# Performance work log

Measured on AMD Instinct MI355X. Metric: run time of the kernel, lower is better.

Reference implementation:

```python
import jax, jax.numpy as jnp
import numpy as np

B, N, E = 2, 32768, 32768
DIM = 3
MP_STEPS = 2
H = 32  # hidden width; original bug: depth == hidden width (range(hidden))


def _ln(x, g, b):
    m = jnp.mean(x, axis=-1, keepdims=True)
    v = jnp.var(x, axis=-1, keepdims=True)
    return (x - m) * jax.lax.rsqrt(v + 1e-5) * g + b


def _mlp(x, Win, bin_, Wh, bh, Wout, bout, lng=None, lnb=None):
    # Linear -> ReLU -> [LN] -> H x (Linear -> ReLU -> [LN]) -> Linear -> ReLU
    h = jax.nn.relu(x @ Win + bin_)
    if lng is not None:
        h = _ln(h, lng[0], lnb[0])
        def body(h, p):
            W, b_, g_, bb = p
            return _ln(jax.nn.relu(h @ W + b_), g_, bb), None
        h, _ = jax.lax.scan(body, h, (Wh, bh, lng[1:], lnb[1:]))
    else:
        def body(h, p):
            W, b_ = p
            return jax.nn.relu(h @ W + b_), None
        h, _ = jax.lax.scan(body, h, (Wh, bh))
    return jax.nn.relu(h @ Wout + bout)


def _mk(key, din, h, dout, ln, pref):
    ks = jax.random.split(key, 3)
    d = {
        pref + 'Win': jax.random.normal(ks[0], (din, h), jnp.float32) / np.sqrt(din).astype(np.float32),
        pref + 'bin': jnp.zeros((h,), jnp.float32),
        pref + 'Wh': jax.random.normal(ks[1], (h, h, h), jnp.float32) / np.sqrt(h).astype(np.float32),
        pref + 'bh': jnp.zeros((h, h), jnp.float32),
        pref + 'Wout': jax.random.normal(ks[2], (h, dout), jnp.float32) / np.sqrt(h).astype(np.float32),
        pref + 'bout': jnp.zeros((dout,), jnp.float32),
    }
    if ln:
        d[pref + 'lng'] = jnp.ones((h + 1, h), jnp.float32)
        d[pref + 'lnb'] = jnp.zeros((h + 1, h), jnp.float32)
    return d


def setup_inputs() -> dict:
    key = jax.random.key(0)
    ks = jax.random.split(key, 10)
    inp = {
        'nodes': jax.random.normal(ks[0], (B, N, 6), jnp.float32),
        'edges': jax.random.normal(ks[1], (B, E, 1), jnp.float32),
        'gvec': jax.random.normal(ks[2], (B,), jnp.float32),
        'senders': jax.random.randint(ks[3], (B, E), 0, N, jnp.int32),
        'receivers': jax.random.randint(ks[4], (B, E), 0, N, jnp.int32),
    }
    inp.update(_mk(ks[5], 6 + 1, H, 16, False, 'ne_'))          # node encoder: node_dim+global
    inp.update(_mk(ks[6], 1 + DIM + 1, H, 16, False, 'ed_'))    # edge encoder: edge_dim+dim+1
    inp.update(_mk(ks[7], 16 + 2 * 16 + 1, H, 16, True, 'pe_')) # edge processor
    inp.update(_mk(ks[8], 16 + 16 + 1, H, 16, True, 'pv_'))     # node processor
    inp.update(_mk(ks[9], 16, H, DIM, False, 'de_'))            # decoder
    return inp


def reference(nodes, edges, gvec, senders, receivers,
              ne_Win, ne_bin, ne_Wh, ne_bh, ne_Wout, ne_bout,
              ed_Win, ed_bin, ed_Wh, ed_bh, ed_Wout, ed_bout,
              pe_Win, pe_bin, pe_Wh, pe_bh, pe_Wout, pe_bout, pe_lng, pe_lnb,
              pv_Win, pv_bin, pv_Wh, pv_bh, pv_Wout, pv_bout, pv_lng, pv_lnb,
              de_Win, de_bin, de_Wh, de_bh, de_Wout, de_bout):
    g_node = jnp.broadcast_to(gvec[:, None, None], (B, N, 1))  # global repeated per node
    g_edge = jnp.broadcast_to(gvec[:, None, None], (B, E, 1))  # global repeated per edge
    x = jnp.concatenate([nodes, g_node], axis=-1)  # [B,N,7]

    # relative edge features from sender/receiver positions (first DIM cols)
    pos = x[..., :DIM]
    si = senders[:, :, None]
    ri = receivers[:, :, None]
    rel = jnp.take_along_axis(pos, si, axis=1) - jnp.take_along_axis(pos, ri, axis=1)  # [B,E,3]
    nrm = jnp.linalg.norm(rel, axis=-1, keepdims=True)
    e_in = jnp.concatenate([edges, rel, nrm], axis=-1)  # [B,E,5]

    ve = _mlp(x, ne_Win, ne_bin, ne_Wh, ne_bh, ne_Wout, ne_bout)       # [B,N,16]
    ee = _mlp(e_in, ed_Win, ed_bin, ed_Wh, ed_bh, ed_Wout, ed_bout)    # [B,E,16]

    seg = jax.vmap(lambda e, r: jax.ops.segment_sum(e, r, num_segments=N))

    for _ in range(MP_STEPS):
        # phi_e: gather sender/receiver node states, concat, edge MLP
        vs = jnp.take_along_axis(ve, si, axis=1)  # [B,E,16]
        vr = jnp.take_along_axis(ve, ri, axis=1)
        ee = _mlp(jnp.concatenate([ee, vs, vr, g_edge], axis=-1),
                  pe_Win, pe_bin, pe_Wh, pe_bh, pe_Wout, pe_bout, pe_lng, pe_lnb)
        # phi_v: scatter-add edge states into receiver nodes, concat, node MLP
        agg = seg(ee, receivers)  # [B,N,16]
        ve = _mlp(jnp.concatenate([agg, ve, g_node], axis=-1),
                  pv_Win, pv_bin, pv_Wh, pv_bh, pv_Wout, pv_bout, pv_lng, pv_lnb)

    return _mlp(ve, de_Win, de_bin, de_Wh, de_bh, de_Wout, de_bout)  # [B,N,3]
```

## Files before the change

kernel.cpp:

```cpp
#include <hip/hip_runtime.h>

#define BB 2
#define NN 32768
#define EN 32768

typedef unsigned int u32;
typedef __attribute__((ext_vector_type(8)))  short bf16x8;
typedef __attribute__((ext_vector_type(2)))  float f32x2;
typedef __attribute__((ext_vector_type(16))) float f32x16;

union U4 { uint4 u; bf16x8 h; };

__device__ __forceinline__ u32 pk2(float lo, float hi) {
    u32 r;
    asm("v_cvt_pk_bf16_f32 %0, %1, %2" : "=v"(r) : "v"(lo), "v"(hi));
    return r;
}

__device__ __forceinline__ float xor32_sum(float x) {
    float y = x;
    asm("v_permlane32_swap_b32 %0, %1" : "+v"(x), "+v"(y));
    return x + y;
}

__device__ __forceinline__ f32x16 MF32(bf16x8 a, bf16x8 b, f32x16 c) {
    return __builtin_amdgcn_mfma_f32_32x32x16_bf16(a, b, c, 0, 0, 0);
}

template<bool LN>
__device__ __forceinline__ void transform32(f32x16 D, bf16x8& B0, bf16x8& B1)
{
    f32x2 p0 = {D[0],D[1]},  p1 = {D[2],D[3]},  p2 = {D[4],D[5]},  p3 = {D[6],D[7]};
    f32x2 p4 = {D[8],D[9]},  p5 = {D[10],D[11]},p6 = {D[12],D[13]},p7 = {D[14],D[15]};
    const f32x2 zz = {0.f, 0.f};
    p0 = __builtin_elementwise_max(p0, zz); p1 = __builtin_elementwise_max(p1, zz);
    p2 = __builtin_elementwise_max(p2, zz); p3 = __builtin_elementwise_max(p3, zz);
    p4 = __builtin_elementwise_max(p4, zz); p5 = __builtin_elementwise_max(p5, zz);
    p6 = __builtin_elementwise_max(p6, zz); p7 = __builtin_elementwise_max(p7, zz);
    if (LN) {
        f32x2 sv = ((p0+p1)+(p2+p3)) + ((p4+p5)+(p6+p7));
        f32x2 ta = __builtin_elementwise_fma(p0,p0,
                   __builtin_elementwise_fma(p1,p1,
                   __builtin_elementwise_fma(p2,p2, p3*p3)));
        f32x2 tb = __builtin_elementwise_fma(p4,p4,
                   __builtin_elementwise_fma(p5,p5,
                   __builtin_elementwise_fma(p6,p6, p7*p7)));
        f32x2 tv = ta + tb;
        float s = xor32_sum(sv.x + sv.y);
        float t = xor32_sum(tv.x + tv.y);
        float mu  = s * (1.f/32.f);
        float var = fmaf(-mu, mu, t * (1.f/32.f));
        float rs  = rsqrtf(var + 1e-5f);
        float nt  = -mu * rs;
        f32x2 rs2 = {rs, rs}, nt2 = {nt, nt};
        p0 = __builtin_elementwise_fma(p0, rs2, nt2);
        p1 = __builtin_elementwise_fma(p1, rs2, nt2);
        p2 = __builtin_elementwise_fma(p2, rs2, nt2);
        p3 = __builtin_elementwise_fma(p3, rs2, nt2);
        p4 = __builtin_elementwise_fma(p4, rs2, nt2);
        p5 = __builtin_elementwise_fma(p5, rs2, nt2);
        p6 = __builtin_elementwise_fma(p6, rs2, nt2);
        p7 = __builtin_elementwise_fma(p7, rs2, nt2);
    }
    U4 c;
    c.u.x = pk2(p0.x,p0.y); c.u.y = pk2(p1.x,p1.y);
    c.u.z = pk2(p2.x,p2.y); c.u.w = pk2(p3.x,p3.y);
    B0 = c.h;
    c.u.x = pk2(p4.x,p4.y); c.u.y = pk2(p5.x,p5.y);
    c.u.z = pk2(p6.x,p6.y); c.u.w = pk2(p7.x,p7.y);
    B1 = c.h;
}

__device__ __forceinline__ f32x16 load_biasC(const float* WB, int base, int h) {
    const float4* p = (const float4*)(WB + base + h*16);
    float4 a = p[0], b = p[1], c = p[2], d = p[3];
    f32x16 C = {a.x,a.y,a.z,a.w, b.x,b.y,b.z,b.w,
                c.x,c.y,c.z,c.w, d.x,d.y,d.z,d.w};
    return C;
}

template<int NT, bool LN>
__device__ __forceinline__ f32x16 mlp32(const bf16x8* bIn,
    const u32* WL, const float* WB, int lane, int h)
{
    constexpr int HB = NT*256;
    constexpr int BO = HB + 16384;
    U4 c;
    f32x16 D = load_biasC(WB, 0, h);
    #pragma unroll
    for (int t = 0; t < NT; ++t) {
        c.u = *(const uint4*)(WL + t*256 + lane*4);
        D = MF32(c.h, bIn[t], D);
    }
    c.u = *(const uint4*)(WL + HB + lane*4);        bf16x8 w0 = c.h;
    c.u = *(const uint4*)(WL + HB + 256 + lane*4);  bf16x8 w1 = c.h;
    c.u = *(const uint4*)(WL + HB + 512 + lane*4);  bf16x8 x0 = c.h;
    c.u = *(const uint4*)(WL + HB + 768 + lane*4);  bf16x8 x1 = c.h;
    f32x16 pb = load_biasC(WB, 32, h);
    bf16x8 B0, B1;
    transform32<LN>(D, B0, B1);
    #pragma unroll 4
    for (int l = 0; l < 32; ++l) {
        const int lp = (l+2 < 32) ? l+2 : 31;
        c.u = *(const uint4*)(WL + HB + lp*512 + lane*4);       bf16x8 nw0 = c.h;
        c.u = *(const uint4*)(WL + HB + lp*512 + 256 + lane*4); bf16x8 nw1 = c.h;
        const int lb_ = (l+1 < 32) ? l+1 : 31;
        f32x16 nb = load_biasC(WB, 32 + lb_*32, h);
        f32x16 E = MF32(w0, B0, pb);
        E = MF32(w1, B1, E);
        transform32<LN>(E, B0, B1);
        w0 = x0; w1 = x1; x0 = nw0; x1 = nw1; pb = nb;
    }
    c.u = *(const uint4*)(WL + BO + lane*4);        bf16x8 o0 = c.h;
    c.u = *(const uint4*)(WL + BO + 256 + lane*4);  bf16x8 o1 = c.h;
    f32x16 Co = load_biasC(WB, 1056, h);
    f32x16 O = MF32(o0, B0, Co);
    O = MF32(o1, B1, O);
    return O;
}

__device__ __forceinline__ void stage_weights32(
    u32* WL, float* WB, const u32* __restrict__ Wp,
    const float* __restrict__ bin, const float* __restrict__ bhid,
    const float* __restrict__ bo, int wtot, int nbo, int tid, int nthr)
{
    const int lane  = tid & 63;
    const int base0 = (tid >> 6) * 256;
    const int step  = (nthr >> 6) * 256;
    for (int C = base0; C < wtot; C += step)
        __builtin_amdgcn_global_load_lds(
            (const __attribute__((address_space(1))) u32*)(Wp + C + lane*4),
            (__attribute__((address_space(3))) u32*)(WL + C), 16, 0, 0);
    for (int i = tid; i < 1088; i += nthr) {
        float v;
        if (i < 32) {
            int w = i, hh = w>>4, r = w&15;
            int f = (r&3) + 8*(r>>2) + 4*hh;
            v = bin[f];
        } else if (i < 1056) {
            int l = (i-32)>>5, w = (i-32)&31, hh = w>>4, r = w&15;
            int f = (r&3) + 8*(r>>2) + 4*hh;
            v = bhid[l*32 + f];
        } else {
            int w = i-1056, hh = w>>4, r = w&15;
            int f = (r&3) + 8*(r>>2) + 4*hh;
            v = (f < nbo) ? bo[f] : 0.f;
        }
        WB[i] = v;
    }
    __syncthreads();
}

__device__ __forceinline__ void pack_body32(
    const float* __restrict__ Win, const float* __restrict__ Wh,
    const float* __restrict__ Wout, const float* __restrict__ lng,
    u32* __restrict__ dst, int din, int dout, int NT, int lb, int tid)
{
    int t = lb * 256 + tid;
    int binW = NT * 256;
    int tot = binW + 16384 + 512;
    if (t >= tot) return;
    float lo, hi;
    if (t < binW) {
        int tt = t>>8, rem = t&255, ln_ = rem>>2, d = rem&3;
        int hh = ln_>>5, m = ln_&31;
        int f0 = 16*tt + 4*hh + 2*(d&1) + 8*(d>>1);
        lo = (f0   < din) ? Win[f0*32 + m]     : 0.f;
        hi = (f0+1 < din) ? Win[(f0+1)*32 + m] : 0.f;
    } else if (t < binW + 16384) {
        int u = t - binW, l = u>>9, v = u&511;
        int tt = v>>8, rem = v&255, ln_ = rem>>2, d = rem&3;
        int hh = ln_>>5, m = ln_&31;
        int f0 = 16*tt + 4*hh + 2*(d&1) + 8*(d>>1);
        lo = Wh[l*1024 + f0*32 + m];
        hi = Wh[l*1024 + (f0+1)*32 + m];
        if (lng) { lo *= lng[l*32 + f0]; hi *= lng[l*32 + f0 + 1]; }
    } else {
        int u = t - binW - 16384;
        int tt = u>>8, rem = u&255, ln_ = rem>>2, d = rem&3;
        int hh = ln_>>5, m = ln_&31;
        int f0 = 16*tt + 4*hh + 2*(d&1) + 8*(d>>1);
        lo = (m < dout) ? Wout[f0*dout + m]     : 0.f;
        hi = (m < dout) ? Wout[(f0+1)*dout + m] : 0.f;
        if (lng) { lo *= lng[1024 + f0]; hi *= lng[1024 + f0 + 1]; }
    }
    dst[t] = pk2(lo, hi);
}

__device__ __forceinline__ void fold_body(
    const float* __restrict__ Wh,   const float* __restrict__ bh,
    const float* __restrict__ Wout, const float* __restrict__ bout,
    const float* __restrict__ lnb,  float* __restrict__ fb, int lb, int tid)
{
    int j = lb * 256 + tid;
    if (j < 1024) {
        int l = j >> 5, jj = j & 31;
        float acc = bh[j];
        #pragma unroll
        for (int k = 0; k < 32; ++k)
            acc = fmaf(lnb[l*32 + k], Wh[l*1024 + k*32 + jj], acc);
        fb[j] = acc;
    } else if (j < 1024 + 16) {
        int jj = j - 1024;
        float acc = bout[jj];
        #pragma unroll
        for (int k = 0; k < 32; ++k)
            acc = fmaf(lnb[1024 + k], Wout[k*16 + jj], acc);
        fb[j] = acc;
    }
}

__global__ __launch_bounds__(256) void prep_kernel(
    const float* ne_Win, const float* ne_Wh, const float* ne_Wout,
    const float* ed_Win, const float* ed_Wh, const float* ed_Wout,
    const float* pe_Win, const float* pe_Wh, const float* pe_Wout,
    const float* pe_lng, const float* pe_lnb, const float* pe_bh, const float* pe_bout,
    const float* pv_Win, const float* pv_Wh, const float* pv_Wout,
    const float* pv_lng, const float* pv_lnb, const float* pv_bh, const float* pv_bout,
    const float* de_Win, const float* de_Wh, const float* de_Wout,
    u32* Wne, u32* Wed, u32* Wpe, u32* Wpv, u32* Wde,
    float* Fpe, float* Fpv)
{
    int bx = blockIdx.x, tid = threadIdx.x;
    if      (bx < 67)  pack_body32(ne_Win, ne_Wh, ne_Wout, nullptr, Wne,  7, 16, 1, bx,       tid);
    else if (bx < 134) pack_body32(ed_Win, ed_Wh, ed_Wout, nullptr, Wed,  5, 16, 1, bx - 67,  tid);
    else if (bx < 204) pack_body32(pe_Win, pe_Wh, pe_Wout, pe_lng,  Wpe, 49, 16, 4, bx - 134, tid);
    else if (bx < 273) pack_body32(pv_Win, pv_Wh, pv_Wout, pv_lng,  Wpv, 33, 16, 3, bx - 204, tid);
    else if (bx < 340) pack_body32(de_Win, de_Wh, de_Wout, nullptr, Wde, 16,  3, 1, bx - 273, tid);
    else if (bx < 345) fold_body(pe_Wh, pe_bh, pe_Wout, pe_bout, pe_lnb, Fpe, bx - 340, tid);
    else               fold_body(pv_Wh, pv_bh, pv_Wout, pv_bout, pv_lnb, Fpv, bx - 345, tid);
}

__device__ __forceinline__ bf16x8 stage_chunk(const float* __restrict__ arr,
                                              size_t e, int h)
{
    const int off = h*4;
    float4 a = *(const float4*)(arr + e*16 + off);
    float4 b = *(const float4*)(arr + e*16 + off + 8);
    U4 c;
    c.u.x = pk2(a.x, a.y); c.u.y = pk2(a.z, a.w);
    c.u.z = pk2(b.x, b.y); c.u.w = pk2(b.z, b.w);
    return c.h;
}

#define WAVE_SETUP \
    const int lane = threadIdx.x & 63; \
    const int wid  = threadIdx.x >> 6; \
    const int el = lane & 31, h = lane >> 5;

__global__ __launch_bounds__(512, 4) void encode_kernel(
    const float* __restrict__ nodes, const float* __restrict__ edges,
    const float* __restrict__ gvec,
    const int* __restrict__ senders, const int* __restrict__ receivers,
    const u32* __restrict__ Wne, const float* __restrict__ ne_bin,
    const float* __restrict__ ne_bh, const float* __restrict__ ne_bout,
    const u32* __restrict__ Wed, const float* __restrict__ ed_bin,
    const float* __restrict__ ed_bh, const float* __restrict__ ed_bout,
    float* __restrict__ ve, float* __restrict__ ee)
{
    __shared__ __align__(16) u32 SL[17152 + 1088];
    u32* WL = SL;
    float* WB = (float*)(SL + 17152);
    WAVE_SETUP
    const bool edge_stage = blockIdx.x >= 256;
    stage_weights32(WL, WB,
                    edge_stage ? Wed : Wne,
                    edge_stage ? ed_bin : ne_bin,
                    edge_stage ? ed_bh : ne_bh,
                    edge_stage ? ed_bout : ne_bout,
                    17152, 16, threadIdx.x, 512);
    const int lb = edge_stage ? (blockIdx.x - 256) : blockIdx.x;
    const int e = (lb*8 + wid)*32 + el;
    const int b = e >> 15;
    bf16x8 a0;
    {
        uint4 w; w.x = 0u; w.y = 0u; w.z = 0u; w.w = 0u;
        if (!edge_stage) {
            if (h == 0) {
                float2 v01 = *(const float2*)(nodes + (size_t)e*6);
                float2 v23 = *(const float2*)(nodes + (size_t)e*6 + 2);
                w.x = pk2(v01.x, v01.y); w.y = pk2(v23.x, v23.y);
            } else {
                float2 v45 = *(const float2*)(nodes + (size_t)e*6 + 4);
                w.x = pk2(v45.x, v45.y); w.y = pk2(gvec[b], 0.f);
            }
        } else {
            int s = senders[e], r = receivers[e];
            const float* ps = nodes + ((size_t)b*NN + s)*6;
            const float* pr = nodes + ((size_t)b*NN + r)*6;
            float2 s01 = *(const float2*)ps; float s2v = ps[2];
            float2 r01 = *(const float2*)pr; float r2v = pr[2];
            float r0 = s01.x - r01.x, r1 = s01.y - r01.y, r2 = s2v - r2v;
            if (h == 0) {
                w.x = pk2(edges[e], r0); w.y = pk2(r1, r2);
            } else {
                w.x = pk2(sqrtf(r0*r0 + r1*r1 + r2*r2), 0.f);
            }
        }
        U4 c; c.u = w; a0 = c.h;
    }
    float* dst = edge_stage ? ee : ve;
    f32x16 O = mlp32<1, false>(&a0, WL, WB, lane, h);
    float4 s1, s2;
    s1.x = fmaxf(O[0], 0.f); s1.y = fmaxf(O[1], 0.f);
    s1.z = fmaxf(O[2], 0.f); s1.w = fmaxf(O[3], 0.f);
    s2.x = fmaxf(O[4], 0.f); s2.y = fmaxf(O[5], 0.f);
    s2.z = fmaxf(O[6], 0.f); s2.w = fmaxf(O[7], 0.f);
    *(float4*)(dst + (size_t)e*16 + h*4)     = s1;
    *(float4*)(dst + (size_t)e*16 + h*4 + 8) = s2;
}

__global__ __launch_bounds__(512, 2) void edge_update_kernel(
    const float* __restrict__ gvec,
    const int* __restrict__ senders, const int* __restrict__ receivers,
    const float* __restrict__ ve, float* __restrict__ ee, float* __restrict__ agg,
    const u32* __restrict__ Wp, const float* __restrict__ bin,
    const float* __restrict__ fb)
{
    __shared__ __align__(16) u32 SL[17920 + 1088 + 8*544];
    u32* WL = SL;
    float* WB = (float*)(SL + 17920);
    WAVE_SETUP
    float* X = (float*)(SL + 19008) + wid*544;
    stage_weights32(WL, WB, Wp, bin, fb, fb + 1024, 17920, 16, threadIdx.x, 512);
    const int e0 = (blockIdx.x*8 + wid)*32;
    const int e  = e0 + el;
    const int b  = e >> 15;
    const int s  = senders[e], r_ = receivers[e];
    bf16x8 a[4];
    a[0] = stage_chunk(ee, (size_t)e, h);
    a[1] = stage_chunk(ve, (size_t)b*NN + s, h);
    a[2] = stage_chunk(ve, (size_t)b*NN + r_, h);
    {
        uint4 w; w.x = (h == 0) ? pk2(gvec[b], 0.f) : 0u;
        w.y = 0u; w.z = 0u; w.w = 0u;
        U4 c; c.u = w; a[3] = c.h;
    }
    f32x16 O = mlp32<4, true>(a, WL, WB, lane, h);
    float4 s1, s2;
    s1.x = fmaxf(O[0], 0.f); s1.y = fmaxf(O[1], 0.f);
    s1.z = fmaxf(O[2], 0.f); s1.w = fmaxf(O[3], 0.f);
    s2.x = fmaxf(O[4], 0.f); s2.y = fmaxf(O[5], 0.f);
    s2.z = fmaxf(O[6], 0.f); s2.w = fmaxf(O[7], 0.f);
    *(float4*)(ee + (size_t)e*16 + h*4)     = s1;
    *(float4*)(ee + (size_t)e*16 + h*4 + 8) = s2;
    *(float4*)(X + el*17 + h*4)     = s1;
    *(float4*)(X + el*17 + h*4 + 8) = s2;
    const int feat = lane & 15;
    #pragma unroll
    for (int rr = 0; rr < 8; ++rr) {
        int m = (lane >> 4)*8 + rr;
        float v = X[m*17 + feat];
        int rc = __shfl(r_, m);
        int eg = e0 + m;
        atomicAdd(agg + ((size_t)(eg >> 15)*NN + rc)*16 + feat, v);
    }
}

template<bool DEC>
__global__ __launch_bounds__(512, 2) void node_update_kernel(
    const float* __restrict__ gvec,
    const float* __restrict__ agg, float* __restrict__ ve,
    const u32* __restrict__ Wp, const float* __restrict__ bin,
    const float* __restrict__ fb,
    const u32* __restrict__ Wde, const float* __restrict__ de_bin,
    const float* __restrict__ de_bh, const float* __restrict__ de_bout,
    float* __restrict__ out)
{
    __shared__ __align__(16) u32 SL[DEC ? (18752 + 17152 + 1088) : 18752];
    u32* WL = SL;
    float* WB = (float*)(SL + 17664);
    u32* WL2 = SL + 18752;
    float* WB2 = (float*)(SL + 18752 + 17152);
    WAVE_SETUP
    stage_weights32(WL, WB, Wp, bin, fb, fb + 1024, 17664, 16, threadIdx.x, 512);
    if (DEC)
        stage_weights32(WL2, WB2, Wde, de_bin, de_bh, de_bout, 17152, 3, threadIdx.x, 512);
    const int e = (blockIdx.x*8 + wid)*32 + el;
    const int b = e >> 15;
    bf16x8 a[3];
    a[0] = stage_chunk(agg, (size_t)e, h);
    a[1] = stage_chunk(ve,  (size_t)e, h);
    {
        uint4 w; w.x = (h == 0) ? pk2(gvec[b], 0.f) : 0u;
        w.y = 0u; w.z = 0u; w.w = 0u;
        U4 c; c.u = w; a[2] = c.h;
    }
    f32x16 O = mlp32<3, true>(a, WL, WB, lane, h);
    if (!DEC) {
        float4 s1, s2;
        s1.x = fmaxf(O[0], 0.f); s1.y = fmaxf(O[1], 0.f);
        s1.z = fmaxf(O[2], 0.f); s1.w = fmaxf(O[3], 0.f);
        s2.x = fmaxf(O[4], 0.f); s2.y = fmaxf(O[5], 0.f);
        s2.z = fmaxf(O[6], 0.f); s2.w = fmaxf(O[7], 0.f);
        *(float4*)(ve + (size_t)e*16 + h*4)     = s1;
        *(float4*)(ve + (size_t)e*16 + h*4 + 8) = s2;
    } else {
        bf16x8 D0, D1;
        transform32<false>(O, D0, D1);
        f32x16 O2 = mlp32<1, false>(&D0, WL2, WB2, lane, h);
        if (h == 0) {
            out[(size_t)e*3 + 0] = fmaxf(O2[0], 0.f);
            out[(size_t)e*3 + 1] = fmaxf(O2[1], 0.f);
            out[(size_t)e*3 + 2] = fmaxf(O2[2], 0.f);
        }
    }
}

extern "C" void kernel_launch(void* const* d_in, const int* in_sizes, int n_in,
                              void* d_out, int out_size, void* d_ws, size_t ws_size,
                              hipStream_t stream)
{
    const float* nodes     = (const float*)d_in[0];
    const float* edges     = (const float*)d_in[1];
    const float* gvec      = (const float*)d_in[2];
    const int*   senders   = (const int*)  d_in[3];
    const int*   receivers = (const int*)  d_in[4];

    const float* ne_Win  = (const float*)d_in[5];
    const float* ne_bin  = (const float*)d_in[6];
    const float* ne_Wh   = (const float*)d_in[7];
    const float* ne_bh   = (const float*)d_in[8];
    const float* ne_Wout = (const float*)d_in[9];
    const float* ne_bout = (const float*)d_in[10];

    const float* ed_Win  = (const float*)d_in[11];
    const float* ed_bin  = (const float*)d_in[12];
    const float* ed_Wh   = (const float*)d_in[13];
    const float* ed_bh   = (const float*)d_in[14];
    const float* ed_Wout = (const float*)d_in[15];
    const float* ed_bout = (const float*)d_in[16];

    const float* pe_Win  = (const float*)d_in[17];
    const float* pe_bin  = (const float*)d_in[18];
    const float* pe_Wh   = (const float*)d_in[19];
    const float* pe_bh   = (const float*)d_in[20];
    const float* pe_Wout = (const float*)d_in[21];
    const float* pe_bout = (const float*)d_in[22];
    const float* pe_lng  = (const float*)d_in[23];
    const float* pe_lnb  = (const float*)d_in[24];

    const float* pv_Win  = (const float*)d_in[25];
    const float* pv_bin  = (const float*)d_in[26];
    const float* pv_Wh   = (const float*)d_in[27];
    const float* pv_bh   = (const float*)d_in[28];
    const float* pv_Wout = (const float*)d_in[29];
    const float* pv_bout = (const float*)d_in[30];
    const float* pv_lng  = (const float*)d_in[31];
    const float* pv_lnb  = (const float*)d_in[32];

    const float* de_Win  = (const float*)d_in[33];
    const float* de_bin  = (const float*)d_in[34];
    const float* de_Wh   = (const float*)d_in[35];
    const float* de_bh   = (const float*)d_in[36];
    const float* de_Wout = (const float*)d_in[37];
    const float* de_bout = (const float*)d_in[38];

    float* ve   = (float*)d_ws;
    float* ee   = ve   + (size_t)1048576;
    float* agg0 = ee   + (size_t)1048576;
    float* agg1 = agg0 + (size_t)1048576;
    u32* Wne = (u32*)(agg1 + (size_t)1048576);
    u32* Wed = Wne + 17152;
    u32* Wpe = Wed + 17152;
    u32* Wpv = Wpe + 17920;
    u32* Wde = Wpv + 17664;
    float* Fpe = (float*)(Wde + 17152);
    float* Fpv = Fpe + 1040;

    prep_kernel<<<350, dim3(256), 0, stream>>>(
        ne_Win, ne_Wh, ne_Wout,
        ed_Win, ed_Wh, ed_Wout,
        pe_Win, pe_Wh, pe_Wout, pe_lng, pe_lnb, pe_bh, pe_bout,
        pv_Win, pv_Wh, pv_Wout, pv_lng, pv_lnb, pv_bh, pv_bout,
        de_Win, de_Wh, de_Wout,
        Wne, Wed, Wpe, Wpv, Wde, Fpe, Fpv);

    hipMemsetAsync(agg0, 0, (size_t)2 * 1048576 * sizeof(float), stream);

    encode_kernel<<<512, dim3(512), 0, stream>>>(nodes, edges, gvec, senders, receivers,
        Wne, ne_bin, ne_bh, ne_bout,
        Wed, ed_bin, ed_bh, ed_bout, ve, ee);

    edge_update_kernel<<<256, dim3(512), 0, stream>>>(gvec, senders, receivers,
        ve, ee, agg0, Wpe, pe_bin, Fpe);
    node_update_kernel<false><<<256, dim3(512), 0, stream>>>(gvec, agg0, ve,
        Wpv, pv_bin, Fpv, Wde, de_bin, de_bh, de_bout, (float*)d_out);
    edge_update_kernel<<<256, dim3(512), 0, stream>>>(gvec, senders, receivers,
        ve, ee, agg1, Wpe, pe_bin, Fpe);
    node_update_kernel<true><<<256, dim3(512), 0, stream>>>(gvec, agg1, ve,
        Wpv, pv_bin, Fpv, Wde, de_bin, de_bh, de_bout, (float*)d_out);
}
```

Baseline: 241.6 us.

## Fuse message-passing kernels into one persistent kernel with grid barriers

```diff
diff --git a/kernel.cpp b/kernel.cpp
--- a/kernel.cpp
+++ b/kernel.cpp
@@ -3,6 +3,7 @@
 #define BB 2
 #define NN 32768
 #define EN 32768
+#define NBLK 256
 
 typedef unsigned int u32;
 typedef __attribute__((ext_vector_type(8)))  short bf16x8;
@@ -72,11 +73,7 @@
 }
 
 __device__ __forceinline__ f32x16 load_biasC(const float* WB, int base, int h) {
-    const float4* p = (const float4*)(WB + base + h*16);
-    float4 a = p[0], b = p[1], c = p[2], d = p[3];
-    f32x16 C = {a.x,a.y,a.z,a.w, b.x,b.y,b.z,b.w,
-                c.x,c.y,c.z,c.w, d.x,d.y,d.z,d.w};
-    return C;
+    return *(const f32x16*)(WB + base + h*16);
 }
 
 template<int NT, bool LN>
@@ -119,19 +116,21 @@
     return O;
 }
 
-__device__ __forceinline__ void stage_weights32(
-    u32* WL, float* WB, const u32* __restrict__ Wp,
-    const float* __restrict__ bin, const float* __restrict__ bhid,
-    const float* __restrict__ bo, int wtot, int nbo, int tid, int nthr)
-{
-    const int lane  = tid & 63;
-    const int base0 = (tid >> 6) * 256;
-    const int step  = (nthr >> 6) * 256;
-    for (int C = base0; C < wtot; C += step)
+__device__ __forceinline__ void stage_dma(u32* WL, const u32* __restrict__ Wp,
+                                          int wtot, int tid)
+{
+    const int lane = tid & 63;
+    for (int C = (tid >> 6)*256; C < wtot; C += 8*256)
         __builtin_amdgcn_global_load_lds(
             (const __attribute__((address_space(1))) u32*)(Wp + C + lane*4),
             (__attribute__((address_space(3))) u32*)(WL + C), 16, 0, 0);
-    for (int i = tid; i < 1088; i += nthr) {
+}
+
+__device__ __forceinline__ void stage_bias(float* WB,
+    const float* __restrict__ bin, const float* __restrict__ bhid,
+    const float* __restrict__ bo, int nbo, int tid)
+{
+    for (int i = tid; i < 1088; i += 512) {
         float v;
         if (i < 32) {
             int w = i, hh = w>>4, r = w&15;
@@ -147,6 +146,34 @@
             v = (f < nbo) ? bo[f] : 0.f;
         }
         WB[i] = v;
+    }
+}
+
+__device__ __forceinline__ void stage_weights32(
+    u32* WL, float* WB, const u32* __restrict__ Wp,
+    const float* __restrict__ bin, const float* __restrict__ bhid,
+    const float* __restrict__ bo, int wtot, int nbo, int tid)
+{
+    stage_dma(WL, Wp, wtot, tid);
+    stage_bias(WB, bin, bhid, bo, nbo, tid);
+    __syncthreads();
+}
+
+__device__ __forceinline__ void gridbar(u32* bar)
+{
+    __threadfence();
+    __syncthreads();
+    if (threadIdx.x == 0) {
+        u32 prev = __hip_atomic_fetch_add(bar, 1u, __ATOMIC_ACQ_REL,
+                                          __HIP_MEMORY_SCOPE_AGENT);
+        if (prev + 1u < NBLK) {
+            u32 v;
+            do {
+                __builtin_amdgcn_s_sleep(2);
+                v = __hip_atomic_load(bar, __ATOMIC_ACQUIRE,
+                                      __HIP_MEMORY_SCOPE_AGENT);
+            } while (v < NBLK);
+        }
     }
     __syncthreads();
 }
@@ -268,7 +295,7 @@
                     edge_stage ? ed_bin : ne_bin,
                     edge_stage ? ed_bh : ne_bh,
                     edge_stage ? ed_bout : ne_bout,
-                    17152, 16, threadIdx.x, 512);
+                    17152, 16, threadIdx.x);
     const int lb = edge_stage ? (blockIdx.x - 256) : blockIdx.x;
     const int e = (lb*8 + wid)*32 + el;
     const int b = e >> 15;
@@ -310,19 +337,13 @@
     *(float4*)(dst + (size_t)e*16 + h*4 + 8) = s2;
 }
 
-__global__ __launch_bounds__(512, 2) void edge_update_kernel(
+__device__ __forceinline__ void eu_phase(
     const float* __restrict__ gvec,
     const int* __restrict__ senders, const int* __restrict__ receivers,
     const float* __restrict__ ve, float* __restrict__ ee, float* __restrict__ agg,
-    const u32* __restrict__ Wp, const float* __restrict__ bin,
-    const float* __restrict__ fb)
-{
-    __shared__ __align__(16) u32 SL[17920 + 1088 + 8*544];
-    u32* WL = SL;
-    float* WB = (float*)(SL + 17920);
-    WAVE_SETUP
-    float* X = (float*)(SL + 19008) + wid*544;
-    stage_weights32(WL, WB, Wp, bin, fb, fb + 1024, 17920, 16, threadIdx.x, 512);
+    const u32* __restrict__ A, const float* __restrict__ WB, float* X,
+    int lane, int wid, int el, int h)
+{
     const int e0 = (blockIdx.x*8 + wid)*32;
     const int e  = e0 + el;
     const int b  = e >> 15;
@@ -336,7 +357,7 @@
         w.y = 0u; w.z = 0u; w.w = 0u;
         U4 c; c.u = w; a[3] = c.h;
     }
-    f32x16 O = mlp32<4, true>(a, WL, WB, lane, h);
+    f32x16 O = mlp32<4, true>(a, A, WB, lane, h);
     float4 s1, s2;
     s1.x = fmaxf(O[0], 0.f); s1.y = fmaxf(O[1], 0.f);
     s1.z = fmaxf(O[2], 0.f); s1.w = fmaxf(O[3], 0.f);
@@ -344,38 +365,45 @@
     s2.z = fmaxf(O[6], 0.f); s2.w = fmaxf(O[7], 0.f);
     *(float4*)(ee + (size_t)e*16 + h*4)     = s1;
     *(float4*)(ee + (size_t)e*16 + h*4 + 8) = s2;
-    *(float4*)(X + el*17 + h*4)     = s1;
-    *(float4*)(X + el*17 + h*4 + 8) = s2;
+    float* Xw = X + (wid & 3)*544;
     const int feat = lane & 15;
-    #pragma unroll
-    for (int rr = 0; rr < 8; ++rr) {
-        int m = (lane >> 4)*8 + rr;
-        float v = X[m*17 + feat];
-        int rc = __shfl(r_, m);
-        int eg = e0 + m;
-        atomicAdd(agg + ((size_t)(eg >> 15)*NN + rc)*16 + feat, v);
+    if (wid < 4) {
+        *(float4*)(Xw + el*17 + h*4)     = s1;
+        *(float4*)(Xw + el*17 + h*4 + 8) = s2;
+        #pragma unroll
+        for (int rr = 0; rr < 8; ++rr) {
+            int m = (lane >> 4)*8 + rr;
+            float v = Xw[m*17 + feat];
+            int rc = __shfl(r_, m);
+            int eg = e0 + m;
+            atomicAdd(agg + ((size_t)(eg >> 15)*NN + rc)*16 + feat, v);
+        }
+    }
+    __syncthreads();
+    if (wid >= 4) {
+        *(float4*)(Xw + el*17 + h*4)     = s1;
+        *(float4*)(Xw + el*17 + h*4 + 8) = s2;
+        #pragma unroll
+        for (int rr = 0; rr < 8; ++rr) {
+            int m = (lane >> 4)*8 + rr;
+            float v = Xw[m*17 + feat];
+            int rc = __shfl(r_, m);
+            int eg = e0 + m;
+            atomicAdd(agg + ((size_t)(eg >> 15)*NN + rc)*16 + feat, v);
+        }
     }
 }
 
 template<bool DEC>
-__global__ __launch_bounds__(512, 2) void node_update_kernel(
+__device__ __forceinline__ void nu_phase(
     const float* __restrict__ gvec,
     const float* __restrict__ agg, float* __restrict__ ve,
-    const u32* __restrict__ Wp, const float* __restrict__ bin,
-    const float* __restrict__ fb,
-    const u32* __restrict__ Wde, const float* __restrict__ de_bin,
-    const float* __restrict__ de_bh, const float* __restrict__ de_bout,
-    float* __restrict__ out)
-{
-    __shared__ __align__(16) u32 SL[DEC ? (18752 + 17152 + 1088) : 18752];
-    u32* WL = SL;
-    float* WB = (float*)(SL + 17664);
-    u32* WL2 = SL + 18752;
-    float* WB2 = (float*)(SL + 18752 + 17152);
-    WAVE_SETUP
-    stage_weights32(WL, WB, Wp, bin, fb, fb + 1024, 17664, 16, threadIdx.x, 512);
-    if (DEC)
-        stage_weights32(WL2, WB2, Wde, de_bin, de_bh, de_bout, 17152, 3, threadIdx.x, 512);
+    const u32* __restrict__ B, float* WB,
+    const u32* __restrict__ A,
+    const float* __restrict__ de_bin, const float* __restrict__ de_bh,
+    const float* __restrict__ de_bout, float* __restrict__ out,
+    int lane, int wid, int el, int h)
+{
     const int e = (blockIdx.x*8 + wid)*32 + el;
     const int b = e >> 15;
     bf16x8 a[3];
@@ -386,7 +414,7 @@
         w.y = 0u; w.z = 0u; w.w = 0u;
         U4 c; c.u = w; a[2] = c.h;
     }
-    f32x16 O = mlp32<3, true>(a, WL, WB, lane, h);
+    f32x16 O = mlp32<3, true>(a, B, WB, lane, h);
     if (!DEC) {
         float4 s1, s2;
         s1.x = fmaxf(O[0], 0.f); s1.y = fmaxf(O[1], 0.f);
@@ -398,13 +426,63 @@
     } else {
         bf16x8 D0, D1;
         transform32<false>(O, D0, D1);
-        f32x16 O2 = mlp32<1, false>(&D0, WL2, WB2, lane, h);
+        __syncthreads();
+        stage_bias(WB, de_bin, de_bh, de_bout, 3, (int)threadIdx.x);
+        __syncthreads();
+        f32x16 O2 = mlp32<1, false>(&D0, A, WB, lane, h);
         if (h == 0) {
             out[(size_t)e*3 + 0] = fmaxf(O2[0], 0.f);
             out[(size_t)e*3 + 1] = fmaxf(O2[1], 0.f);
             out[(size_t)e*3 + 2] = fmaxf(O2[2], 0.f);
         }
     }
+}
+
+__global__ __launch_bounds__(512, 2) void mp_fused_kernel(
+    const float* __restrict__ gvec,
+    const int* __restrict__ senders, const int* __restrict__ receivers,
+    float* __restrict__ ve, float* __restrict__ ee,
+    float* __restrict__ agg0, float* __restrict__ agg1,
+    const u32* __restrict__ Wpe, const float* __restrict__ pe_bin,
+    const float* __restrict__ Fpe,
+    const u32* __restrict__ Wpv, const float* __restrict__ pv_bin,
+    const float* __restrict__ Fpv,
+    const u32* __restrict__ Wde, const float* __restrict__ de_bin,
+    const float* __restrict__ de_bh, const float* __restrict__ de_bout,
+    u32* __restrict__ bar, float* __restrict__ out)
+{
+    __shared__ __align__(16) u32 SL[38848];
+    u32* A   = SL;
+    u32* B   = SL + 17920;
+    float* WB = (float*)(SL + 35584);
+    float* X  = (float*)(SL + 36672);
+    WAVE_SETUP
+    const int tid = threadIdx.x;
+
+    stage_dma(A, Wpe, 17920, tid);
+    stage_dma(B, Wpv, 17664, tid);
+    stage_bias(WB, pe_bin, Fpe, Fpe + 1024, 16, tid);
+    __syncthreads();
+
+    eu_phase(gvec, senders, receivers, ve, ee, agg0, A, WB, X, lane, wid, el, h);
+    gridbar(bar + 0);
+
+    stage_bias(WB, pv_bin, Fpv, Fpv + 1024, 16, tid);
+    __syncthreads();
+    nu_phase<false>(gvec, agg0, ve, B, WB, A, de_bin, de_bh, de_bout, out,
+                    lane, wid, el, h);
+    gridbar(bar + 1);
+
+    stage_bias(WB, pe_bin, Fpe, Fpe + 1024, 16, tid);
+    __syncthreads();
+    eu_phase(gvec, senders, receivers, ve, ee, agg1, A, WB, X, lane, wid, el, h);
+    gridbar(bar + 2);
+
+    stage_dma(A, Wde, 17152, tid);
+    stage_bias(WB, pv_bin, Fpv, Fpv + 1024, 16, tid);
+    __syncthreads();
+    nu_phase<true>(gvec, agg1, ve, B, WB, A, de_bin, de_bh, de_bout, out,
+                   lane, wid, el, h);
 }
 
 extern "C" void kernel_launch(void* const* d_in, const int* in_sizes, int n_in,
@@ -460,7 +538,8 @@
     float* ee   = ve   + (size_t)1048576;
     float* agg0 = ee   + (size_t)1048576;
     float* agg1 = agg0 + (size_t)1048576;
-    u32* Wne = (u32*)(agg1 + (size_t)1048576);
+    u32* bar = (u32*)(agg1 + (size_t)1048576);
+    u32* Wne = bar + 16;
     u32* Wed = Wne + 17152;
     u32* Wpe = Wed + 17152;
     u32* Wpv = Wpe + 17920;
@@ -476,18 +555,16 @@
         de_Win, de_Wh, de_Wout,
         Wne, Wed, Wpe, Wpv, Wde, Fpe, Fpv);
 
-    hipMemsetAsync(agg0, 0, (size_t)2 * 1048576 * sizeof(float), stream);
+    hipMemsetAsync(agg0, 0, (size_t)2 * 1048576 * sizeof(float) + 64, stream);
 
     encode_kernel<<<512, dim3(512), 0, stream>>>(nodes, edges, gvec, senders, receivers,
         Wne, ne_bin, ne_bh, ne_bout,
         Wed, ed_bin, ed_bh, ed_bout, ve, ee);
 
-    edge_update_kernel<<<256, dim3(512), 0, stream>>>(gvec, senders, receivers,
-        ve, ee, agg0, Wpe, pe_bin, Fpe);
-    node_update_kernel<false><<<256, dim3(512), 0, stream>>>(gvec, agg0, ve,
-        Wpv, pv_bin, Fpv, Wde, de_bin, de_bh, de_bout, (float*)d_out);
-    edge_update_kernel<<<256, dim3(512), 0, stream>>>(gvec, senders, receivers,
-        ve, ee, agg1, Wpe, pe_bin, Fpe);
-    node_update_kernel<true><<<256, dim3(512), 0, stream>>>(gvec, agg1, ve,
-        Wpv, pv_bin, Fpv, Wde, de_bin, de_bh, de_bout, (float*)d_out);
-}
+    mp_fused_kernel<<<NBLK, dim3(512), 0, stream>>>(gvec, senders, receivers,
+        ve, ee, agg0, agg1,
+        Wpe, pe_bin, Fpe,
+        Wpv, pv_bin, Fpv,
+        Wde, de_bin, de_bh, de_bout,
+        bar, (float*)d_out);
+}
```

Result: slower. 425.3 us (+76.0%).

## Process two 32-row tiles per wave to interleave independent MFMA chains

Applied to the files above, without the earlier changes.

```diff
diff --git a/kernel.cpp b/kernel.cpp
--- a/kernel.cpp
+++ b/kernel.cpp
@@ -72,65 +72,71 @@
 }
 
 __device__ __forceinline__ f32x16 load_biasC(const float* WB, int base, int h) {
-    const float4* p = (const float4*)(WB + base + h*16);
-    float4 a = p[0], b = p[1], c = p[2], d = p[3];
-    f32x16 C = {a.x,a.y,a.z,a.w, b.x,b.y,b.z,b.w,
-                c.x,c.y,c.z,c.w, d.x,d.y,d.z,d.w};
-    return C;
+    return *(const f32x16*)(WB + base + h*16);
 }
 
 template<int NT, bool LN>
-__device__ __forceinline__ f32x16 mlp32(const bf16x8* bIn,
-    const u32* WL, const float* WB, int lane, int h)
+__device__ __forceinline__ void mlp32x2(const bf16x8* aA, const bf16x8* aB,
+    f32x16& OA, f32x16& OB, const u32* WL, const float* WB, int lane, int h)
 {
     constexpr int HB = NT*256;
     constexpr int BO = HB + 16384;
     U4 c;
-    f32x16 D = load_biasC(WB, 0, h);
+    f32x16 DA = load_biasC(WB, 0, h);
+    f32x16 DB = DA;
     #pragma unroll
     for (int t = 0; t < NT; ++t) {
         c.u = *(const uint4*)(WL + t*256 + lane*4);
-        D = MF32(c.h, bIn[t], D);
+        DA = MF32(c.h, aA[t], DA);
+        DB = MF32(c.h, aB[t], DB);
     }
     c.u = *(const uint4*)(WL + HB + lane*4);        bf16x8 w0 = c.h;
     c.u = *(const uint4*)(WL + HB + 256 + lane*4);  bf16x8 w1 = c.h;
     c.u = *(const uint4*)(WL + HB + 512 + lane*4);  bf16x8 x0 = c.h;
     c.u = *(const uint4*)(WL + HB + 768 + lane*4);  bf16x8 x1 = c.h;
     f32x16 pb = load_biasC(WB, 32, h);
-    bf16x8 B0, B1;
-    transform32<LN>(D, B0, B1);
-    #pragma unroll 4
+    bf16x8 A0, A1, B0, B1;
+    transform32<LN>(DA, A0, A1);
+    transform32<LN>(DB, B0, B1);
+    #pragma unroll 2
     for (int l = 0; l < 32; ++l) {
         const int lp = (l+2 < 32) ? l+2 : 31;
         c.u = *(const uint4*)(WL + HB + lp*512 + lane*4);       bf16x8 nw0 = c.h;
         c.u = *(const uint4*)(WL + HB + lp*512 + 256 + lane*4); bf16x8 nw1 = c.h;
         const int lb_ = (l+1 < 32) ? l+1 : 31;
         f32x16 nb = load_biasC(WB, 32 + lb_*32, h);
-        f32x16 E = MF32(w0, B0, pb);
-        E = MF32(w1, B1, E);
-        transform32<LN>(E, B0, B1);
+        f32x16 EA = MF32(w0, A0, pb);
+        EA = MF32(w1, A1, EA);
+        f32x16 EB = MF32(w0, B0, pb);
+        EB = MF32(w1, B1, EB);
+        transform32<LN>(EA, A0, A1);
+        transform32<LN>(EB, B0, B1);
         w0 = x0; w1 = x1; x0 = nw0; x1 = nw1; pb = nb;
     }
     c.u = *(const uint4*)(WL + BO + lane*4);        bf16x8 o0 = c.h;
     c.u = *(const uint4*)(WL + BO + 256 + lane*4);  bf16x8 o1 = c.h;
     f32x16 Co = load_biasC(WB, 1056, h);
-    f32x16 O = MF32(o0, B0, Co);
-    O = MF32(o1, B1, O);
-    return O;
-}
-
-__device__ __forceinline__ void stage_weights32(
-    u32* WL, float* WB, const u32* __restrict__ Wp,
-    const float* __restrict__ bin, const float* __restrict__ bhid,
-    const float* __restrict__ bo, int wtot, int nbo, int tid, int nthr)
-{
-    const int lane  = tid & 63;
-    const int base0 = (tid >> 6) * 256;
-    const int step  = (nthr >> 6) * 256;
-    for (int C = base0; C < wtot; C += step)
+    OA = MF32(o0, A0, Co);
+    OA = MF32(o1, A1, OA);
+    OB = MF32(o0, B0, Co);
+    OB = MF32(o1, B1, OB);
+}
+
+__device__ __forceinline__ void stage_dma(u32* WL, const u32* __restrict__ Wp,
+                                          int wtot, int tid, int nthr)
+{
+    const int lane = tid & 63;
+    const int step = (nthr >> 6) * 256;
+    for (int C = (tid >> 6)*256; C < wtot; C += step)
         __builtin_amdgcn_global_load_lds(
             (const __attribute__((address_space(1))) u32*)(Wp + C + lane*4),
             (__attribute__((address_space(3))) u32*)(WL + C), 16, 0, 0);
+}
+
+__device__ __forceinline__ void stage_bias(float* WB,
+    const float* __restrict__ bin, const float* __restrict__ bhid,
+    const float* __restrict__ bo, int nbo, int tid, int nthr)
+{
     for (int i = tid; i < 1088; i += nthr) {
         float v;
         if (i < 32) {
@@ -148,6 +154,15 @@
         }
         WB[i] = v;
     }
+}
+
+__device__ __forceinline__ void stage_weights32(
+    u32* WL, float* WB, const u32* __restrict__ Wp,
+    const float* __restrict__ bin, const float* __restrict__ bhid,
+    const float* __restrict__ bo, int wtot, int nbo, int tid, int nthr)
+{
+    stage_dma(WL, Wp, wtot, tid, nthr);
+    stage_bias(WB, bin, bhid, bo, nbo, tid, nthr);
     __syncthreads();
 }
 
@@ -243,12 +258,55 @@
     return c.h;
 }
 
+__device__ __forceinline__ void store_relu(float* __restrict__ dst, size_t e,
+                                           int h, f32x16 O)
+{
+    float4 s1, s2;
+    s1.x = fmaxf(O[0], 0.f); s1.y = fmaxf(O[1], 0.f);
+    s1.z = fmaxf(O[2], 0.f); s1.w = fmaxf(O[3], 0.f);
+    s2.x = fmaxf(O[4], 0.f); s2.y = fmaxf(O[5], 0.f);
+    s2.z = fmaxf(O[6], 0.f); s2.w = fmaxf(O[7], 0.f);
+    *(float4*)(dst + e*16 + h*4)     = s1;
+    *(float4*)(dst + e*16 + h*4 + 8) = s2;
+}
+
 #define WAVE_SETUP \
     const int lane = threadIdx.x & 63; \
     const int wid  = threadIdx.x >> 6; \
     const int el = lane & 31, h = lane >> 5;
 
-__global__ __launch_bounds__(512, 4) void encode_kernel(
+__device__ __forceinline__ bf16x8 enc_input(bool es, int e, int b,
+    const float* __restrict__ nodes, const float* __restrict__ edges,
+    const float* __restrict__ gvec,
+    const int* __restrict__ senders, const int* __restrict__ receivers, int h)
+{
+    uint4 w; w.x = 0u; w.y = 0u; w.z = 0u; w.w = 0u;
+    if (!es) {
+        if (h == 0) {
+            float2 v01 = *(const float2*)(nodes + (size_t)e*6);
+            float2 v23 = *(const float2*)(nodes + (size_t)e*6 + 2);
+            w.x = pk2(v01.x, v01.y); w.y = pk2(v23.x, v23.y);
+        } else {
+            float2 v45 = *(const float2*)(nodes + (size_t)e*6 + 4);
+            w.x = pk2(v45.x, v45.y); w.y = pk2(gvec[b], 0.f);
+        }
+    } else {
+        int s = senders[e], r = receivers[e];
+        const float* ps = nodes + ((size_t)b*NN + s)*6;
+        const float* pr = nodes + ((size_t)b*NN + r)*6;
+        float2 s01 = *(const float2*)ps; float s2v = ps[2];
+        float2 r01 = *(const float2*)pr; float r2v = pr[2];
+        float r0 = s01.x - r01.x, r1 = s01.y - r01.y, r2 = s2v - r2v;
+        if (h == 0) {
+            w.x = pk2(edges[e], r0); w.y = pk2(r1, r2);
+        } else {
+            w.x = pk2(sqrtf(r0*r0 + r1*r1 + r2*r2), 0.f);
+        }
+    }
+    U4 c; c.u = w; return c.h;
+}
+
+__global__ __launch_bounds__(256, 2) void encode_kernel(
     const float* __restrict__ nodes, const float* __restrict__ edges,
     const float* __restrict__ gvec,
     const int* __restrict__ senders, const int* __restrict__ receivers,
@@ -258,107 +316,90 @@
     const float* __restrict__ ed_bh, const float* __restrict__ ed_bout,
     float* __restrict__ ve, float* __restrict__ ee)
 {
-    __shared__ __align__(16) u32 SL[17152 + 1088];
+    __shared__ __align__(64) u32 SL[17152 + 1088];
     u32* WL = SL;
     float* WB = (float*)(SL + 17152);
     WAVE_SETUP
-    const bool edge_stage = blockIdx.x >= 256;
+    const bool es = blockIdx.x >= 256;
     stage_weights32(WL, WB,
-                    edge_stage ? Wed : Wne,
-                    edge_stage ? ed_bin : ne_bin,
-                    edge_stage ? ed_bh : ne_bh,
-                    edge_stage ? ed_bout : ne_bout,
-                    17152, 16, threadIdx.x, 512);
-    const int lb = edge_stage ? (blockIdx.x - 256) : blockIdx.x;
-    const int e = (lb*8 + wid)*32 + el;
-    const int b = e >> 15;
-    bf16x8 a0;
-    {
-        uint4 w; w.x = 0u; w.y = 0u; w.z = 0u; w.w = 0u;
-        if (!edge_stage) {
-            if (h == 0) {
-                float2 v01 = *(const float2*)(nodes + (size_t)e*6);
-                float2 v23 = *(const float2*)(nodes + (size_t)e*6 + 2);
-                w.x = pk2(v01.x, v01.y); w.y = pk2(v23.x, v23.y);
-            } else {
-                float2 v45 = *(const float2*)(nodes + (size_t)e*6 + 4);
-                w.x = pk2(v45.x, v45.y); w.y = pk2(gvec[b], 0.f);
-            }
-        } else {
-            int s = senders[e], r = receivers[e];
-            const float* ps = nodes + ((size_t)b*NN + s)*6;
-            const float* pr = nodes + ((size_t)b*NN + r)*6;
-            float2 s01 = *(const float2*)ps; float s2v = ps[2];
-            float2 r01 = *(const float2*)pr; float r2v = pr[2];
-            float r0 = s01.x - r01.x, r1 = s01.y - r01.y, r2 = s2v - r2v;
-            if (h == 0) {
-                w.x = pk2(edges[e], r0); w.y = pk2(r1, r2);
-            } else {
-                w.x = pk2(sqrtf(r0*r0 + r1*r1 + r2*r2), 0.f);
-            }
-        }
-        U4 c; c.u = w; a0 = c.h;
-    }
-    float* dst = edge_stage ? ee : ve;
-    f32x16 O = mlp32<1, false>(&a0, WL, WB, lane, h);
+                    es ? Wed : Wne, es ? ed_bin : ne_bin,
+                    es ? ed_bh : ne_bh, es ? ed_bout : ne_bout,
+                    17152, 16, threadIdx.x, 256);
+    const int lb = es ? (blockIdx.x - 256) : blockIdx.x;
+    const int eA = (lb*8 + wid*2)*32 + el;
+    const int eB = eA + 32;
+    const int b = eA >> 15;
+    bf16x8 aA = enc_input(es, eA, b, nodes, edges, gvec, senders, receivers, h);
+    bf16x8 aB = enc_input(es, eB, b, nodes, edges, gvec, senders, receivers, h);
+    float* dst = es ? ee : ve;
+    f32x16 OA, OB;
+    mlp32x2<1, false>(&aA, &aB, OA, OB, WL, WB, lane, h);
+    store_relu(dst, (size_t)eA, h, OA);
+    store_relu(dst, (size_t)eB, h, OB);
+}
+
+__device__ __forceinline__ void scatter_agg(float* Xw, f32x16 O,
+    int r_, int e0, float* __restrict__ agg, int lane, int el, int h)
+{
     float4 s1, s2;
     s1.x = fmaxf(O[0], 0.f); s1.y = fmaxf(O[1], 0.f);
     s1.z = fmaxf(O[2], 0.f); s1.w = fmaxf(O[3], 0.f);
     s2.x = fmaxf(O[4], 0.f); s2.y = fmaxf(O[5], 0.f);
     s2.z = fmaxf(O[6], 0.f); s2.w = fmaxf(O[7], 0.f);
-    *(float4*)(dst + (size_t)e*16 + h*4)     = s1;
-    *(float4*)(dst + (size_t)e*16 + h*4 + 8) = s2;
-}
-
-__global__ __launch_bounds__(512, 2) void edge_update_kernel(
+    *(float4*)(Xw + el*17 + h*4)     = s1;
+    *(float4*)(Xw + el*17 + h*4 + 8) = s2;
+    const int feat = lane & 15;
+    #pragma unroll
+    for (int rr = 0; rr < 8; ++rr) {
+        int m = (lane >> 4)*8 + rr;
+        float v = Xw[m*17 + feat];
+        int rc = __shfl(r_, m);
+        int eg = e0 + m;
+        atomicAdd(agg + ((size_t)(eg >> 15)*NN + rc)*16 + feat, v);
+    }
+}
+
+__global__ __launch_bounds__(256, 1) void edge_update_kernel(
     const float* __restrict__ gvec,
     const int* __restrict__ senders, const int* __restrict__ receivers,
     const float* __restrict__ ve, float* __restrict__ ee, float* __restrict__ agg,
     const u32* __restrict__ Wp, const float* __restrict__ bin,
     const float* __restrict__ fb)
 {
-    __shared__ __align__(16) u32 SL[17920 + 1088 + 8*544];
+    __shared__ __align__(64) u32 SL[17920 + 1088 + 4*544];
     u32* WL = SL;
     float* WB = (float*)(SL + 17920);
     WAVE_SETUP
-    float* X = (float*)(SL + 19008) + wid*544;
-    stage_weights32(WL, WB, Wp, bin, fb, fb + 1024, 17920, 16, threadIdx.x, 512);
-    const int e0 = (blockIdx.x*8 + wid)*32;
-    const int e  = e0 + el;
-    const int b  = e >> 15;
-    const int s  = senders[e], r_ = receivers[e];
-    bf16x8 a[4];
-    a[0] = stage_chunk(ee, (size_t)e, h);
-    a[1] = stage_chunk(ve, (size_t)b*NN + s, h);
-    a[2] = stage_chunk(ve, (size_t)b*NN + r_, h);
+    float* Xw = (float*)(SL + 19008) + wid*544;
+    stage_weights32(WL, WB, Wp, bin, fb, fb + 1024, 17920, 16, threadIdx.x, 256);
+    const int e0A = (blockIdx.x*8 + wid*2)*32;
+    const int e0B = e0A + 32;
+    const int eA = e0A + el, eB = e0B + el;
+    const int b  = eA >> 15;
+    const int sA = senders[eA], rA = receivers[eA];
+    const int sB = senders[eB], rB = receivers[eB];
+    bf16x8 aA[4], aB[4];
+    aA[0] = stage_chunk(ee, (size_t)eA, h);
+    aB[0] = stage_chunk(ee, (size_t)eB, h);
+    aA[1] = stage_chunk(ve, (size_t)b*NN + sA, h);
+    aB[1] = stage_chunk(ve, (size_t)b*NN + sB, h);
+    aA[2] = stage_chunk(ve, (size_t)b*NN + rA, h);
+    aB[2] = stage_chunk(ve, (size_t)b*NN + rB, h);
     {
         uint4 w; w.x = (h == 0) ? pk2(gvec[b], 0.f) : 0u;
         w.y = 0u; w.z = 0u; w.w = 0u;
-        U4 c; c.u = w; a[3] = c.h;
-    }
-    f32x16 O = mlp32<4, true>(a, WL, WB, lane, h);
-    float4 s1, s2;
-    s1.x = fmaxf(O[0], 0.f); s1.y = fmaxf(O[1], 0.f);
-    s1.z = fmaxf(O[2], 0.f); s1.w = fmaxf(O[3], 0.f);
-    s2.x = fmaxf(O[4], 0.f); s2.y = fmaxf(O[5], 0.f);
-    s2.z = fmaxf(O[6], 0.f); s2.w = fmaxf(O[7], 0.f);
-    *(float4*)(ee + (size_t)e*16 + h*4)     = s1;
-    *(float4*)(ee + (size_t)e*16 + h*4 + 8) = s2;
-    *(float4*)(X + el*17 + h*4)     = s1;
-    *(float4*)(X + el*17 + h*4 + 8) = s2;
-    const int feat = lane & 15;
-    #pragma unroll
-    for (int rr = 0; rr < 8; ++rr) {
-        int m = (lane >> 4)*8 + rr;
-        float v = X[m*17 + feat];
-        int rc = __shfl(r_, m);
-        int eg = e0 + m;
-        atomicAdd(agg + ((size_t)(eg >> 15)*NN + rc)*16 + feat, v);
-    }
+        U4 c; c.u = w; aA[3] = c.h; aB[3] = c.h;
+    }
+    f32x16 OA, OB;
+    mlp32x2<4, true>(aA, aB, OA, OB, WL, WB, lane, h);
+    store_relu(ee, (size_t)eA, h, OA);
+    store_relu(ee, (size_t)eB, h, OB);
+    scatter_agg(Xw, OA, rA, e0A, agg, lane, el, h);
+    scatter_agg(Xw, OB, rB, e0B, agg, lane, el, h);
 }
 
 template<bool DEC>
-__global__ __launch_bounds__(512, 2) void node_update_kernel(
+__global__ __launch_bounds__(256, 1) void node_update_kernel(
     const float* __restrict__ gvec,
     const float* __restrict__ agg, float* __restrict__ ve,
     const u32* __restrict__ Wp, const float* __restrict__ bin,
@@ -367,42 +408,45 @@
     const float* __restrict__ de_bh, const float* __restrict__ de_bout,
     float* __restrict__ out)
 {
-    __shared__ __align__(16) u32 SL[DEC ? (18752 + 17152 + 1088) : 18752];
+    __shared__ __align__(64) u32 SL[17664 + 1088];
     u32* WL = SL;
     float* WB = (float*)(SL + 17664);
-    u32* WL2 = SL + 18752;
-    float* WB2 = (float*)(SL + 18752 + 17152);
     WAVE_SETUP
-    stage_weights32(WL, WB, Wp, bin, fb, fb + 1024, 17664, 16, threadIdx.x, 512);
-    if (DEC)
-        stage_weights32(WL2, WB2, Wde, de_bin, de_bh, de_bout, 17152, 3, threadIdx.x, 512);
-    const int e = (blockIdx.x*8 + wid)*32 + el;
-    const int b = e >> 15;
-    bf16x8 a[3];
-    a[0] = stage_chunk(agg, (size_t)e, h);
-    a[1] = stage_chunk(ve,  (size_t)e, h);
+    stage_weights32(WL, WB, Wp, bin, fb, fb + 1024, 17664, 16, threadIdx.x, 256);
+    const int eA = (blockIdx.x*8 + wid*2)*32 + el;
+    const int eB = eA + 32;
+    const int b = eA >> 15;
+    bf16x8 aA[3], aB[3];
+    aA[0] = stage_chunk(agg, (size_t)eA, h);
+    aB[0] = stage_chunk(agg, (size_t)eB, h);
+    aA[1] = stage_chunk(ve,  (size_t)eA, h);
+    aB[1] = stage_chunk(ve,  (size_t)eB, h);
     {
         uint4 w; w.x = (h == 0) ? pk2(gvec[b], 0.f) : 0u;
         w.y = 0u; w.z = 0u; w.w = 0u;
-        U4 c; c.u = w; a[2] = c.h;
-    }
-    f32x16 O = mlp32<3, true>(a, WL, WB, lane, h);
+        U4 c; c.u = w; aA[2] = c.h; aB[2] = c.h;
+    }
+    f32x16 OA, OB;
+    mlp32x2<3, true>(aA, aB, OA, OB, WL, WB, lane, h);
     if (!DEC) {
-        float4 s1, s2;
-        s1.x = fmaxf(O[0], 0.f); s1.y = fmaxf(O[1], 0.f);
-        s1.z = fmaxf(O[2], 0.f); s1.w = fmaxf(O[3], 0.f);
-        s2.x = fmaxf(O[4], 0.f); s2.y = fmaxf(O[5], 0.f);
-        s2.z = fmaxf(O[6], 0.f); s2.w = fmaxf(O[7], 0.f);
-        *(float4*)(ve + (size_t)e*16 + h*4)     = s1;
-        *(float4*)(ve + (size_t)e*16 + h*4 + 8) = s2;
+        store_relu(ve, (size_t)eA, h, OA);
+        store_relu(ve, (size_t)eB, h, OB);
     } else {
-        bf16x8 D0, D1;
-        transform32<false>(O, D0, D1);
-        f32x16 O2 = mlp32<1, false>(&D0, WL2, WB2, lane, h);
+        bf16x8 dA0, dA1, dB0, dB1;
+        transform32<false>(OA, dA0, dA1);
+        transform32<false>(OB, dB0, dB1);
+        __syncthreads();
+        stage_weights32(WL, WB, Wde, de_bin, de_bh, de_bout, 17152, 3,
+                        threadIdx.x, 256);
+        f32x16 QA, QB;
+        mlp32x2<1, false>(&dA0, &dB0, QA, QB, WL, WB, lane, h);
         if (h == 0) {
-            out[(size_t)e*3 + 0] = fmaxf(O2[0], 0.f);
-            out[(size_t)e*3 + 1] = fmaxf(O2[1], 0.f);
-            out[(size_t)e*3 + 2] = fmaxf(O2[2], 0.f);
+            out[(size_t)eA*3 + 0] = fmaxf(QA[0], 0.f);
+            out[(size_t)eA*3 + 1] = fmaxf(QA[1], 0.f);
+            out[(size_t)eA*3 + 2] = fmaxf(QA[2], 0.f);
+            out[(size_t)eB*3 + 0] = fmaxf(QB[0], 0.f);
+            out[(size_t)eB*3 + 1] = fmaxf(QB[1], 0.f);
+            out[(size_t)eB*3 + 2] = fmaxf(QB[2], 0.f);
         }
     }
 }
@@ -478,16 +522,16 @@
 
     hipMemsetAsync(agg0, 0, (size_t)2 * 1048576 * sizeof(float), stream);
 
-    encode_kernel<<<512, dim3(512), 0, stream>>>(nodes, edges, gvec, senders, receivers,
+    encode_kernel<<<512, dim3(256), 0, stream>>>(nodes, edges, gvec, senders, receivers,
         Wne, ne_bin, ne_bh, ne_bout,
         Wed, ed_bin, ed_bh, ed_bout, ve, ee);
 
-    edge_update_kernel<<<256, dim3(512), 0, stream>>>(gvec, senders, receivers,
+    edge_update_kernel<<<256, dim3(256), 0, stream>>>(gvec, senders, receivers,
         ve, ee, agg0, Wpe, pe_bin, Fpe);
-    node_update_kernel<false><<<256, dim3(512), 0, stream>>>(gvec, agg0, ve,
+    node_update_kernel<false><<<256, dim3(256), 0, stream>>>(gvec, agg0, ve,
         Wpv, pv_bin, Fpv, Wde, de_bin, de_bh, de_bout, (float*)d_out);
-    edge_update_kernel<<<256, dim3(512), 0, stream>>>(gvec, senders, receivers,
+    edge_update_kernel<<<256, dim3(256), 0, stream>>>(gvec, senders, receivers,
         ve, ee, agg1, Wpe, pe_bin, Fpe);
-    node_update_kernel<true><<<256, dim3(512), 0, stream>>>(gvec, agg1, ve,
+    node_update_kernel<true><<<256, dim3(256), 0, stream>>>(gvec, agg1, ve,
         Wpv, pv_bin, Fpv, Wde, de_bin, de_bh, de_bout, (float*)d_out);
 }
```

Result: slower. 259.6 us (+7.4%).
